# Kernel tuning notes

Measured on AMD Instinct MI355X. Metric: run time of the kernel, lower is better.

The kernel has to match this reference:

```python
import jax, jax.numpy as jnp
import numpy as np

B, S, D, P, H = 32, 1024, 512, 720, 4   # batch, seq_len (=codebook_size), enc_in, pred_len, heads
COMMIT_W, ORTHO_W = 1.0, 0.8


def setup_inputs() -> dict:
    key = jax.random.key(0)
    ks = jax.random.split(key, 6)
    return {
        "x": jax.random.normal(ks[0], (B, S, D), jnp.float32),
        "w_in": jax.random.normal(ks[1], (H * D, D), jnp.float32) * 0.02,   # project_in: dim -> heads*dim
        "b_in": jnp.zeros((H * D,), jnp.float32),
        "embed": jax.random.normal(ks[2], (H, S, D), jnp.float32),          # per-head codebook [h, C, d]
        "w_out": jax.random.normal(ks[3], (D, H * D), jnp.float32) * 0.02,  # project_out: heads*dim -> dim
        "b_out": jnp.zeros((D,), jnp.float32),
        "w_lin": jax.random.normal(ks[4], (P, S), jnp.float32) * 0.02,      # Linear over time axis
        "b_lin": jnp.zeros((P,), jnp.float32),
    }


def reference(x, w_in, b_in, embed, w_out, b_out, w_lin, b_lin):
    C = embed.shape[1]
    # Normalization: subtract last timestep (detached)
    seq_last = jax.lax.stop_gradient(x[:, -1:, :])          # [B,1,D]
    x0 = x - seq_last                                       # [B,S,D]

    # --- VectorQuantize ---
    xi = x0 @ w_in.T + b_in                                 # [B,S,H*D] project_in
    # 'b n (h d) -> h (b n) d' (separate codebook per head)
    f = xi.reshape(B, S, H, D).transpose(2, 0, 1, 3).reshape(H, B * S, D)
    # squared-euclidean distances to codes: [H, B*S, C]
    d2 = (jnp.sum(f * f, -1, keepdims=True)
          - 2.0 * jnp.einsum('hnd,hcd->hnc', f, embed)
          + jnp.sum(embed * embed, -1)[:, None, :])
    ind = jnp.argmin(d2, axis=-1)                           # [H, B*S]
    q = jnp.take_along_axis(embed, ind[:, :, None], axis=1)  # gather -> [H, B*S, D]

    # commitment loss (learnable codebook => quantize NOT detached)
    commit_loss = jnp.mean((q - f) ** 2)
    # orthogonal regularization on full codebook
    normed = embed / jnp.linalg.norm(embed, axis=-1, keepdims=True)
    cs = jnp.einsum('hid,hjd->hij', normed, normed)         # [H,C,C]
    ortho_loss = jnp.sum(cs ** 2) / (H * C * C) - 1.0 / C
    loss = COMMIT_W * commit_loss + ORTHO_W * ortho_loss

    # straight-through estimator
    q_st = f + jax.lax.stop_gradient(q - f)
    # 'h (b n) d -> b n (h d)'
    qo = q_st.reshape(H, B, S, D).transpose(1, 2, 0, 3).reshape(B, S, H * D)
    quantized = qo @ w_out.T + b_out                        # [B,S,D] project_out

    # Linear over the time axis: permute(0,2,1) -> Linear(S->P) -> permute back
    y = jnp.einsum('bnd,pn->bpd', quantized, w_lin) + b_lin[None, :, None]
    y = y + seq_last                                        # [B,P,D]

    indices = ind.reshape(H, B, S).transpose(1, 2, 0)       # [B,S,H]
    return y, indices, loss
```

## Files before the change

kernel.cpp:

```cpp
#include <hip/hip_runtime.h>
#include <stdint.h>

typedef unsigned int u32;
typedef unsigned long long u64;
typedef _Float16 f16;
typedef __attribute__((ext_vector_type(8))) _Float16 f16x8;
typedef __attribute__((ext_vector_type(4))) _Float16 f16x4;
typedef __attribute__((ext_vector_type(2))) _Float16 f16x2;
typedef __attribute__((ext_vector_type(4))) float f32x4;

#define MFMA16(a, b, c) __builtin_amdgcn_mfma_f32_16x16x32_f16((a), (b), (c), 0, 0, 0)
#define MARGIN 2.0f
#define WAITV(n) asm volatile("s_waitcnt vmcnt(" #n ")" ::: "memory")

__device__ __forceinline__ u32 ford(float x) { u32 u = __float_as_uint(x); return (u & 0x80000000u) ? ~u : (u | 0x80000000u); }
__device__ __forceinline__ float iford(u32 v) { u32 u = (v & 0x80000000u) ? (v & 0x7FFFFFFFu) : ~v; return __uint_as_float(u); }
__device__ __forceinline__ int xswz(int i, int n) { return (i & 7) * (n >> 3) + (i >> 3); }

typedef __attribute__((address_space(1))) const unsigned char ga_t;
typedef __attribute__((address_space(3))) unsigned char la_t;
__device__ __forceinline__ void gl16(const void* g, void* l) {
  __builtin_amdgcn_global_load_lds((ga_t*)g, (la_t*)l, 16, 0, 0);
}

__device__ __forceinline__ void stgp(const f16* g, int kt, char* sdst, int tid) {
#pragma unroll
  for (int it = 0; it < 2; ++it) {
    const int u = (tid + (it << 9)) << 4;
    const int r = u >> 7, sl = (u >> 4) & 7;
    const char* src = (const char*)g + (size_t)r * 1024 + ((size_t)kt << 7) +
                      (size_t)((sl ^ (r & 7)) << 4);
    gl16(src, sdst + u);
  }
}

__device__ __forceinline__ f16x8 rdf(const char* bb, int pb, int rr, int ks, int lane) {
  return *(const f16x8*)(bb + pb + rr * 128 +
                         ((((ks << 2) + (lane >> 4)) ^ (rr & 7)) << 4));
}

template <bool ISK1>
__global__ __launch_bounds__(512, 1) void gemm8(
    const f16* __restrict__ A0, const f16* __restrict__ A1,
    const f16* __restrict__ B0, const f16* __restrict__ B1,
    int chrows, void* __restrict__ out0, void* __restrict__ out1,
    const float* __restrict__ bias, const float* __restrict__ aux) {
  __shared__ char lds[131072 + (ISK1 ? 0 : 4096)];
  const int tid = threadIdx.x;
  const int lane = tid & 63, wid = tid >> 6;
  const int wm = wid >> 2, wn = wid & 3;

  int blkm, blkn, z = 0;
  {
    const int s = xswz(blockIdx.x, gridDim.x);
    if constexpr (ISK1) { blkn = s & 15; blkm = s >> 4; }
    else {
      const int bph = (chrows >> 8) << 2;
      z = s / bph;
      const int rem = s - z * bph;
      blkm = rem >> 2; blkn = rem & 3;
    }
  }

  if constexpr (!ISK1) {
    ((int*)(lds + 131072))[tid] = 0;
    ((int*)(lds + 131072))[tid + 512] = 0;
  }

  const f16 *p0, *p1, *p2, *p3;
  if constexpr (ISK1) {
    p0 = A0 + (size_t)blkm * 65536;
    p1 = A1 + (size_t)blkm * 65536;
    p2 = B0 + (size_t)blkn * 65536;
    p3 = B1 + (size_t)blkn * 65536;
  } else {
    p0 = A0 + ((size_t)z * chrows + (size_t)blkm * 256) * 512;
    p1 = p0 + 65536;
    p2 = B0 + (size_t)z * 524288 + (size_t)blkn * 131072;
    p3 = p2 + 65536;
  }

  constexpr int NACC = ISK1 ? 8 : 32;
  f32x4 acc[NACC];
#pragma unroll
  for (int i = 0; i < NACC; ++i) acc[i] = f32x4{0.f, 0.f, 0.f, 0.f};

  stgp(p0, 0, lds + 0, tid);
  stgp(p1, 0, lds + 16384, tid);
  stgp(p2, 0, lds + 32768, tid);
  stgp(p3, 0, lds + 49152, tid);

#pragma unroll
  for (int kc = 0; kc < 8; ++kc) {
    const char* bb = lds + (kc & 1) * 65536;
    char* nb = lds + ((kc + 1) & 1) * 65536;
    __builtin_amdgcn_s_barrier();
    if (kc + 1 < 8) {
      stgp(p0, kc + 1, nb + 0, tid);
      stgp(p1, kc + 1, nb + 16384, tid);
      stgp(p2, kc + 1, nb + 32768, tid);
      stgp(p3, kc + 1, nb + 49152, tid);
      WAITV(8);
    } else {
      WAITV(0);
    }
    __builtin_amdgcn_s_barrier();

    if constexpr (!ISK1) {
      f16x8 a[4][2], b[4][2];
      const int pbA = wm * 16384;
      const int pbB = 32768 + (wn >> 1) * 16384;
      const int rB = (wn & 1) * 64 + (lane & 15);
#pragma unroll
      for (int mt = 0; mt < 4; ++mt)
#pragma unroll
        for (int ks = 0; ks < 2; ++ks) a[mt][ks] = rdf(bb, pbA, mt * 16 + (lane & 15), ks, lane);
#pragma unroll
      for (int nt = 0; nt < 2; ++nt)
#pragma unroll
        for (int ks = 0; ks < 2; ++ks) b[nt][ks] = rdf(bb, pbB, rB + nt * 16, ks, lane);
      __builtin_amdgcn_s_setprio(1);
#pragma unroll
      for (int nt = 0; nt < 2; ++nt)
#pragma unroll
        for (int mt = 0; mt < 4; ++mt)
#pragma unroll
          for (int ks = 0; ks < 2; ++ks) acc[mt * 4 + nt] = MFMA16(a[mt][ks], b[nt][ks], acc[mt * 4 + nt]);
      __builtin_amdgcn_s_setprio(0);
#pragma unroll
      for (int nt = 2; nt < 4; ++nt)
#pragma unroll
        for (int ks = 0; ks < 2; ++ks) b[nt][ks] = rdf(bb, pbB, rB + nt * 16, ks, lane);
      __builtin_amdgcn_s_setprio(1);
#pragma unroll
      for (int nt = 2; nt < 4; ++nt)
#pragma unroll
        for (int mt = 0; mt < 4; ++mt)
#pragma unroll
          for (int ks = 0; ks < 2; ++ks) acc[mt * 4 + nt] = MFMA16(a[mt][ks], b[nt][ks], acc[mt * 4 + nt]);
      __builtin_amdgcn_s_setprio(0);
#pragma unroll
      for (int mt = 0; mt < 4; ++mt)
#pragma unroll
        for (int ks = 0; ks < 2; ++ks) a[mt][ks] = rdf(bb, pbA, (mt + 4) * 16 + (lane & 15), ks, lane);
      __builtin_amdgcn_s_setprio(1);
#pragma unroll
      for (int nt = 2; nt < 4; ++nt)
#pragma unroll
        for (int mt = 0; mt < 4; ++mt)
#pragma unroll
          for (int ks = 0; ks < 2; ++ks) acc[(mt + 4) * 4 + nt] = MFMA16(a[mt][ks], b[nt][ks], acc[(mt + 4) * 4 + nt]);
      __builtin_amdgcn_s_setprio(0);
      __builtin_amdgcn_s_setprio(1);
#pragma unroll
      for (int nt = 0; nt < 2; ++nt)
#pragma unroll
        for (int mt = 0; mt < 4; ++mt)
#pragma unroll
          for (int ks = 0; ks < 2; ++ks) acc[(mt + 4) * 4 + nt] = MFMA16(a[mt][ks], b[nt][ks], acc[(mt + 4) * 4 + nt]);
      __builtin_amdgcn_s_setprio(0);
    } else {
      f16x8 ah[2][2], al[2][2], bh[2][2], bl[2][2];
      const int rA = wm * 64 + (lane & 15);
      const int rB = wn * 32 + (lane & 15);
#pragma unroll
      for (int mt = 0; mt < 2; ++mt)
#pragma unroll
        for (int ks = 0; ks < 2; ++ks) {
          ah[mt][ks] = rdf(bb, 0, rA + mt * 16, ks, lane);
          al[mt][ks] = rdf(bb, 16384, rA + mt * 16, ks, lane);
        }
#pragma unroll
      for (int ks = 0; ks < 2; ++ks) {
        bh[0][ks] = rdf(bb, 32768, rB, ks, lane);
        bl[0][ks] = rdf(bb, 49152, rB, ks, lane);
      }
      __builtin_amdgcn_s_setprio(1);
#pragma unroll
      for (int mt = 0; mt < 2; ++mt)
#pragma unroll
        for (int ks = 0; ks < 2; ++ks) {
          acc[mt * 2] = MFMA16(al[mt][ks], bh[0][ks], acc[mt * 2]);
          acc[mt * 2] = MFMA16(ah[mt][ks], bl[0][ks], acc[mt * 2]);
          acc[mt * 2] = MFMA16(ah[mt][ks], bh[0][ks], acc[mt * 2]);
        }
      __builtin_amdgcn_s_setprio(0);
#pragma unroll
      for (int ks = 0; ks < 2; ++ks) {
        bh[1][ks] = rdf(bb, 32768, rB + 16, ks, lane);
        bl[1][ks] = rdf(bb, 49152, rB + 16, ks, lane);
      }
      __builtin_amdgcn_s_setprio(1);
#pragma unroll
      for (int mt = 0; mt < 2; ++mt)
#pragma unroll
        for (int ks = 0; ks < 2; ++ks) {
          acc[mt * 2 + 1] = MFMA16(al[mt][ks], bh[1][ks], acc[mt * 2 + 1]);
          acc[mt * 2 + 1] = MFMA16(ah[mt][ks], bl[1][ks], acc[mt * 2 + 1]);
          acc[mt * 2 + 1] = MFMA16(ah[mt][ks], bh[1][ks], acc[mt * 2 + 1]);
        }
      __builtin_amdgcn_s_setprio(0);
#pragma unroll
      for (int mt = 0; mt < 2; ++mt)
#pragma unroll
        for (int ks = 0; ks < 2; ++ks) {
          ah[mt][ks] = rdf(bb, 0, rA + (mt + 2) * 16, ks, lane);
          al[mt][ks] = rdf(bb, 16384, rA + (mt + 2) * 16, ks, lane);
        }
      __builtin_amdgcn_s_setprio(1);
#pragma unroll
      for (int mt = 0; mt < 2; ++mt)
#pragma unroll
        for (int ks = 0; ks < 2; ++ks) {
          acc[(mt + 2) * 2 + 1] = MFMA16(al[mt][ks], bh[1][ks], acc[(mt + 2) * 2 + 1]);
          acc[(mt + 2) * 2 + 1] = MFMA16(ah[mt][ks], bl[1][ks], acc[(mt + 2) * 2 + 1]);
          acc[(mt + 2) * 2 + 1] = MFMA16(ah[mt][ks], bh[1][ks], acc[(mt + 2) * 2 + 1]);
        }
      __builtin_amdgcn_s_setprio(0);
      __builtin_amdgcn_s_setprio(1);
#pragma unroll
      for (int mt = 0; mt < 2; ++mt)
#pragma unroll
        for (int ks = 0; ks < 2; ++ks) {
          acc[(mt + 2) * 2] = MFMA16(al[mt][ks], bh[0][ks], acc[(mt + 2) * 2]);
          acc[(mt + 2) * 2] = MFMA16(ah[mt][ks], bl[0][ks], acc[(mt + 2) * 2]);
          acc[(mt + 2) * 2] = MFMA16(ah[mt][ks], bh[0][ks], acc[(mt + 2) * 2]);
        }
      __builtin_amdgcn_s_setprio(0);
    }
  }

  if constexpr (ISK1) {
    f16* fh = (f16*)out0;
    f16* fl = (f16*)out1;
#pragma unroll
    for (int nt = 0; nt < 2; ++nt) {
      const int gc = blkn * 128 + wn * 32 + nt * 16 + (lane & 15);
      const float bv = bias[gc];
      const int h = gc >> 9, d = gc & 511;
#pragma unroll
      for (int mt = 0; mt < 4; ++mt)
#pragma unroll
        for (int r = 0; r < 4; ++r) {
          const int grow = blkm * 128 + wm * 64 + mt * 16 + ((lane >> 4) << 2) + r;
          const float v = acc[mt * 2 + nt][r] * 6.103515625e-05f + bv;
          const f16 hv = (f16)v;
          const size_t off = ((size_t)h * chrows + grow) * 512 + d;
          fh[off] = hv;
          fl[off] = (f16)(v - (float)hv);
        }
    }
  } else {
    int* cntL = (int*)(lds + 131072);
    u64* candG = (u64*)out0;
    const int h = z;
    float escol[4];
    int cc[4];
#pragma unroll
    for (int nt = 0; nt < 4; ++nt) {
      cc[nt] = blkn * 256 + wn * 64 + nt * 16 + (lane & 15);
      escol[nt] = aux[h * 1024 + cc[nt]];
    }
#pragma unroll
    for (int mt = 0; mt < 8; ++mt)
#pragma unroll
      for (int r = 0; r < 4; ++r) {
        const int row_l = wm * 128 + mt * 16 + ((lane >> 4) << 2) + r;
        float vals[4];
        float mn = 3.4e38f;
#pragma unroll
        for (int nt = 0; nt < 4; ++nt) {
          const float v = escol[nt] - 2.0f * acc[mt * 4 + nt][r];
          vals[nt] = v;
          mn = fminf(mn, v);
        }
#pragma unroll
        for (int o = 1; o < 16; o <<= 1) mn = fminf(mn, __shfl_xor(mn, o));
        const float lim = mn + MARGIN;
#pragma unroll
        for (int nt = 0; nt < 4; ++nt)
          if (vals[nt] <= lim) {
            const int p = atomicAdd(&cntL[row_l * 4 + wn], 1);
            if (p < 4) {
              const size_t grow = (size_t)blkm * 256 + row_l;
              candG[((size_t)h * chrows + grow) * 64 + blkn * 16 + wn * 4 + p] =
                  ((u64)ford(vals[nt]) << 32) | (u32)cc[nt];
            }
          }
      }
  }
}

template <int LDK>
__device__ __forceinline__ void stg8k(const f16* gRowBase, int ktile, char* sdst, int tid) {
#pragma unroll
  for (int it = 0; it < 2; ++it) {
    const int u = (tid + (it << 8)) << 4;
    const int r = u >> 6, s = (u >> 4) & 3;
    const char* src = (const char*)gRowBase + (size_t)r * (LDK * 2) + ((size_t)ktile << 6) +
                      (size_t)((s ^ ((r >> 1) & 3)) << 4);
    gl16(src, sdst + u);
  }
}

template <int MODE>
__global__ __launch_bounds__(256, 3) void gemm2(
    const f16* __restrict__ Ah, const f16* __restrict__ Bh,
    void* __restrict__ out0, const float* __restrict__ bias,
    const float* __restrict__ aux, u64* __restrict__ slots) {
  constexpr int LDK = (MODE == 2 || MODE == 4) ? 1024 : 512;
  constexpr int D = 3;
  constexpr int KT = (MODE == 2 || MODE == 4) ? 32 : 16;
  constexpr int BUF = 16384;
  __shared__ char lds[D * BUF];

  const int tid = threadIdx.x;
  const int lane = tid & 63, wid = tid >> 6;
  const int wm = wid >> 1, wn = wid & 1;

  int blkm, blkn, z = 0;
  {
    const int s = xswz(blockIdx.x, gridDim.x);
    if constexpr (MODE == 1) { blkn = s & 3; blkm = s >> 2; z = blkm >> 3; }
    else if constexpr (MODE == 2) { blkn = s & 3; blkm = (s >> 2) & 3; z = s >> 4; }
    else { const int r2 = s % 24; blkm = r2 % 6; blkn = r2 / 6; z = s / 24; }
  }

  const f16 *Ab, *Bb;
  if constexpr (MODE == 1) {
    Ab = Ah + (size_t)blkm * 65536;
    Bb = Bh + (size_t)z * 262144 + (size_t)blkn * 65536;
  } else if constexpr (MODE == 2) {
    Ab = Ah + (size_t)z * 524288 + (size_t)blkm * 131072;
    Bb = Bh + (size_t)z * 524288 + (size_t)blkn * 131072;
  } else {
    Ab = Ah + (size_t)blkm * 131072;
    Bb = Bh + (size_t)z * 524288 + (size_t)blkn * 131072;
  }

  f32x4 acc[4][4];
#pragma unroll
  for (int i = 0; i < 4; ++i)
#pragma unroll
    for (int j = 0; j < 4; ++j) acc[i][j] = f32x4{0.f, 0.f, 0.f, 0.f};

  auto stage = [&](int kt, char* nb) {
    stg8k<LDK>(Ab, kt, nb, tid);
    stg8k<LDK>(Bb, kt, nb + 8192, tid);
  };
#pragma unroll
  for (int d = 0; d < D - 1; ++d) stage(d, lds + d * BUF);

#pragma unroll
  for (int kc = 0; kc < KT; ++kc) {
    if (kc + D - 1 < KT) stage(kc + D - 1, lds + ((kc + D - 1) % D) * BUF);
    const int nf = KT - 1 - kc;
    if (nf >= 2) WAITV(8);
    else if (nf == 1) WAITV(4);
    else WAITV(0);
    __builtin_amdgcn_s_barrier();
    const char* cbuf = lds + (kc % D) * BUF;
    f16x8 ah[4];
#pragma unroll
    for (int mt = 0; mt < 4; ++mt) {
      const int rr = wm * 64 + mt * 16 + (lane & 15);
      ah[mt] = *(const f16x8*)(cbuf + rr * 64 + (((lane >> 4) ^ ((rr >> 1) & 3)) << 4));
    }
    __builtin_amdgcn_s_setprio(1);
#pragma unroll
    for (int nt = 0; nt < 4; ++nt) {
      const int rn = wn * 64 + nt * 16 + (lane & 15);
      const f16x8 bh = *(const f16x8*)(cbuf + 8192 + rn * 64 + (((lane >> 4) ^ ((rn >> 1) & 3)) << 4));
#pragma unroll
      for (int mt = 0; mt < 4; ++mt) acc[mt][nt] = MFMA16(ah[mt], bh, acc[mt][nt]);
    }
    __builtin_amdgcn_s_setprio(0);
    __builtin_amdgcn_s_barrier();
  }

  if constexpr (MODE == 1) {
    f16* o = (f16*)out0;
#pragma unroll
    for (int nt = 0; nt < 4; ++nt) {
      const int gc = blkn * 128 + wn * 64 + nt * 16 + (lane & 15);
#pragma unroll
      for (int mt = 0; mt < 4; ++mt)
#pragma unroll
        for (int r = 0; r < 4; ++r) {
          const size_t grow = (size_t)blkm * 128 + wm * 64 + mt * 16 + ((lane >> 4) << 2) + r;
          o[grow * 512 + gc] = (f16)acc[mt][nt][r];
        }
    }
  } else if constexpr (MODE == 2) {
    float ssum = 0.f;
#pragma unroll
    for (int mt = 0; mt < 4; ++mt)
#pragma unroll
      for (int nt = 0; nt < 4; ++nt)
#pragma unroll
        for (int r = 0; r < 4; ++r) ssum += acc[mt][nt][r] * acc[mt][nt][r];
#pragma unroll
    for (int o = 1; o < 64; o <<= 1) ssum += __shfl_xor(ssum, o);
    float* wp = (float*)lds;
    __syncthreads();
    if (lane == 0) wp[wid] = ssum;
    __syncthreads();
    if (tid == 0) {
      const float p = wp[0] + wp[1] + wp[2] + wp[3];
      atomicAdd(slots + (blockIdx.x & 63), (u64)llrintf(p * 16777216.f));
    }
  } else {
    float* oy = (float*)out0 + (size_t)z * 368640;
    const float* xseq = aux + (size_t)z * 524288 + 523776;
    float sl[4];
    int gd[4];
#pragma unroll
    for (int nt = 0; nt < 4; ++nt) {
      gd[nt] = blkn * 128 + wn * 64 + nt * 16 + (lane & 15);
      sl[nt] = xseq[gd[nt]];
    }
#pragma unroll
    for (int mt = 0; mt < 4; ++mt)
#pragma unroll
      for (int r = 0; r < 4; ++r) {
        const int p = blkm * 128 + wm * 64 + mt * 16 + ((lane >> 4) << 2) + r;
        if (p < 720) {
          const float bp = bias[p];
#pragma unroll
          for (int nt = 0; nt < 4; ++nt) oy[(size_t)p * 512 + gd[nt]] = acc[mt][nt][r] + bp + sl[nt];
        }
      }
  }
}

__global__ __launch_bounds__(256, 4) void rescore_k(
    const u64* __restrict__ candG, const f16* __restrict__ fh,
    const f16* __restrict__ fl, const float* __restrict__ embed,
    int n0, int shCH,
    int* __restrict__ indw, float* __restrict__ indout, u64* __restrict__ cslots) {
  const int tid = threadIdx.x, lane = tid & 63, wid = tid >> 6;
  const int r = blockIdx.x * 4 + wid;
  const int h = r >> shCH, row = r & ((1 << shCH) - 1);
  u64 cu = candG[(size_t)r * 64 + lane];
  u64 mn = cu;
#pragma unroll
  for (int o = 1; o < 64; o <<= 1) { const u64 t = __shfl_xor(mn, o); if (t < mn) mn = t; }
  const float lim = iford((u32)(mn >> 32)) + MARGIN;
  const bool pass = iford((u32)(cu >> 32)) <= lim;
  u64 mask = __ballot(pass);
  float fv[8];
  {
    const size_t fo = (size_t)r * 512 + lane * 8;
    const f16x8 hv = *(const f16x8*)(fh + fo);
    const f16x8 lv = *(const f16x8*)(fl + fo);
#pragma unroll
    for (int j = 0; j < 8; ++j) fv[j] = (float)hv[j] + (float)lv[j];
  }
  double bestd = 1e300;
  int bestc = 0x7FFFFFFF;
  while (mask) {
    const int src = __ffsll((unsigned long long)mask) - 1;
    mask &= mask - 1;
    const int c = (int)(u32)__shfl(cu, src);
    const float* e = embed + ((size_t)h * 1024 + c) * 512 + lane * 8;
    const float4 e0 = *(const float4*)e, e1 = *(const float4*)(e + 4);
    const float ev[8] = {e0.x, e0.y, e0.z, e0.w, e1.x, e1.y, e1.z, e1.w};
    double sd = 0.0;
#pragma unroll
    for (int j = 0; j < 8; ++j) { const double d = (double)fv[j] - (double)ev[j]; sd += d * d; }
#pragma unroll
    for (int o = 1; o < 64; o <<= 1) sd += __shfl_xor(sd, o);
    if (sd < bestd || (sd == bestd && c < bestc)) { bestd = sd; bestc = c; }
  }
  if (lane == 0) {
    const int n = n0 + row;
    indw[(size_t)n * 4 + h] = bestc;
    indout[(size_t)n * 4 + h] = (float)bestc;
    atomicAdd(cslots + (blockIdx.x & 255), (u64)llrint(bestd * 65536.0));
  }
}

__global__ __launch_bounds__(256) void quantize_qT(
    const int* __restrict__ indw, const f16* __restrict__ Ep,
    const float* __restrict__ b_out, f16* __restrict__ qT) {
  const int tid = threadIdx.x;
  const int b = blockIdx.x >> 4, s0 = (blockIdx.x & 15) << 6;
  __shared__ int inds[64][4];
  inds[tid >> 2][tid & 3] = indw[(size_t)(b * 1024 + s0 + (tid >> 2)) * 4 + (tid & 3)];
  __syncthreads();
  const int d0 = tid * 2;
  const float ba0 = b_out[d0], ba1 = b_out[d0 + 1];
  u32 r0[32], r1[32];
  f16 t0 = (f16)0.f, t1 = (f16)0.f;
#pragma unroll
  for (int ss = 0; ss < 64; ++ss) {
    float a0 = ba0, a1 = ba1;
#pragma unroll
    for (int h = 0; h < 4; ++h) {
      const int c = inds[ss][h];
      const f16x2 p = *(const f16x2*)(Ep + (((size_t)h * 1024 + c) * 512 + d0));
      a0 += (float)p[0];
      a1 += (float)p[1];
    }
    const f16 q0 = (f16)a0, q1 = (f16)a1;
    if (ss & 1) {
      f16x2 w0; w0[0] = t0; w0[1] = q0; __builtin_memcpy(&r0[ss >> 1], &w0, 4);
      f16x2 w1; w1[0] = t1; w1[1] = q1; __builtin_memcpy(&r1[ss >> 1], &w1, 4);
    } else { t0 = q0; t1 = q1; }
  }
  const size_t o0 = ((size_t)b * 512 + d0) * 1024 + s0;
#pragma unroll
  for (int i = 0; i < 8; ++i) {
    uint4 v; v.x = r0[4 * i]; v.y = r0[4 * i + 1]; v.z = r0[4 * i + 2]; v.w = r0[4 * i + 3];
    *(uint4*)(qT + o0 + (size_t)i * 8) = v;
  }
  const size_t o1 = o0 + 1024;
#pragma unroll
  for (int i = 0; i < 8; ++i) {
    uint4 v; v.x = r1[4 * i]; v.y = r1[4 * i + 1]; v.z = r1[4 * i + 2]; v.w = r1[4 * i + 3];
    *(uint4*)(qT + o1 + (size_t)i * 8) = v;
  }
}

__global__ __launch_bounds__(256) void prep_x0(const float* __restrict__ x, int n0,
                                               f16* __restrict__ ht, f16* __restrict__ lt) {
  const int id = blockIdx.x * 256 + threadIdx.x;
  const int k8 = id & 63, r = id >> 6;
  const int n = n0 + r, b = n >> 10;
  const float* ap = x + (size_t)n * 512 + k8 * 8;
  const float* sp = x + (size_t)b * 524288 + 523776 + k8 * 8;
  const float4 a0 = *(const float4*)ap, a1 = *(const float4*)(ap + 4);
  const float4 s0 = *(const float4*)sp, s1 = *(const float4*)(sp + 4);
  const float v[8] = {(a0.x - s0.x) * 16.f, (a0.y - s0.y) * 16.f, (a0.z - s0.z) * 16.f,
                      (a0.w - s0.w) * 16.f, (a1.x - s1.x) * 16.f, (a1.y - s1.y) * 16.f,
                      (a1.z - s1.z) * 16.f, (a1.w - s1.w) * 16.f};
  f16x8 hv, lv;
#pragma unroll
  for (int j = 0; j < 8; ++j) { const f16 h = (f16)v[j]; hv[j] = h; lv[j] = (f16)(v[j] - (float)h); }
  const size_t off = (size_t)r * 512 + k8 * 8;
  *(f16x8*)(ht + off) = hv;
  *(f16x8*)(lt + off) = lv;
}

__global__ __launch_bounds__(256) void prep_win(const float* __restrict__ src,
                                                f16* __restrict__ hi, f16* __restrict__ lo) {
  const size_t e = ((size_t)blockIdx.x * 256 + threadIdx.x) * 4;
  const float4 v = *(const float4*)(src + e);
  const float w[4] = {v.x * 1024.f, v.y * 1024.f, v.z * 1024.f, v.w * 1024.f};
  f16x4 hv, lv;
#pragma unroll
  for (int j = 0; j < 4; ++j) { const f16 h = (f16)w[j]; hv[j] = h; lv[j] = (f16)(w[j] - (float)h); }
  *(f16x4*)(hi + e) = hv;
  *(f16x4*)(lo + e) = lv;
}

__global__ __launch_bounds__(256) void prep_embed_k(const float* __restrict__ em,
                                                    f16* __restrict__ ef,
                                                    float* __restrict__ esq,
                                                    float* __restrict__ invn) {
  const int tid = threadIdx.x, lane = tid & 63, wid = tid >> 6;
  const int row = blockIdx.x * 4 + wid;
  const float* er = em + (size_t)row * 512 + lane * 8;
  const float4 a = *(const float4*)er, b = *(const float4*)(er + 4);
  f16x8 v;
  v[0] = (f16)a.x; v[1] = (f16)a.y; v[2] = (f16)a.z; v[3] = (f16)a.w;
  v[4] = (f16)b.x; v[5] = (f16)b.y; v[6] = (f16)b.z; v[7] = (f16)b.w;
  *(f16x8*)(ef + (size_t)row * 512 + lane * 8) = v;
  float s = a.x * a.x + a.y * a.y + a.z * a.z + a.w * a.w +
            b.x * b.x + b.y * b.y + b.z * b.z + b.w * b.w;
#pragma unroll
  for (int o = 1; o < 64; o <<= 1) s += __shfl_xor(s, o);
  if (lane == 0) { esq[row] = s; invn[row] = 1.0f / sqrtf(s); }
}

__global__ __launch_bounds__(256) void prep_wout(const float* __restrict__ src,
                                                 f16* __restrict__ dst) {
  const int id = blockIdx.x * 256 + threadIdx.x;
  const int k8 = id & 63, rg = id >> 6;
  const int d = rg & 511, h = rg >> 9;
  const float* ap = src + (size_t)d * 2048 + h * 512 + k8 * 8;
  const float4 a0 = *(const float4*)ap, a1 = *(const float4*)(ap + 4);
  f16x8 v;
  v[0] = (f16)a0.x; v[1] = (f16)a0.y; v[2] = (f16)a0.z; v[3] = (f16)a0.w;
  v[4] = (f16)a1.x; v[5] = (f16)a1.y; v[6] = (f16)a1.z; v[7] = (f16)a1.w;
  *(f16x8*)(dst + (size_t)h * 262144 + (size_t)d * 512 + k8 * 8) = v;
}

__global__ __launch_bounds__(256) void prep_wlin(const float* __restrict__ src,
                                                 f16* __restrict__ dst) {
  const int id = blockIdx.x * 256 + threadIdx.x;
  const int k8 = id & 127, row = id >> 7;
  float4 a0 = {0.f, 0.f, 0.f, 0.f}, a1 = a0;
  if (row < 720) {
    const float* ap = src + (size_t)row * 1024 + k8 * 8;
    a0 = *(const float4*)ap;
    a1 = *(const float4*)(ap + 4);
  }
  f16x8 v;
  v[0] = (f16)a0.x; v[1] = (f16)a0.y; v[2] = (f16)a0.z; v[3] = (f16)a0.w;
  v[4] = (f16)a1.x; v[5] = (f16)a1.y; v[6] = (f16)a1.z; v[7] = (f16)a1.w;
  *(f16x8*)(dst + (size_t)row * 1024 + k8 * 8) = v;
}

__global__ __launch_bounds__(256) void prep_normT(const float* __restrict__ em,
                                                  const float* __restrict__ invn,
                                                  f16* __restrict__ nT) {
  __shared__ float t[64 * 65];
  const int tid = threadIdx.x;
  const int bx = blockIdx.x;
  const int h = bx >> 7, rem = bx & 127, cb = rem >> 3, db = rem & 7;
  const int c0 = cb * 64, d0 = db * 64;
  const int j = tid & 63, i0 = tid >> 6;
#pragma unroll
  for (int p = 0; p < 16; ++p) {
    const int i = p * 4 + i0;
    t[i * 65 + j] = em[(size_t)h * 524288 + (size_t)(c0 + i) * 512 + d0 + j] * invn[h * 1024 + c0 + i];
  }
  __syncthreads();
#pragma unroll
  for (int p = 0; p < 16; ++p) {
    const int i = p * 4 + i0;
    nT[(size_t)h * 524288 + (size_t)(d0 + i) * 1024 + c0 + j] = (f16)t[j * 65 + i];
  }
}

__global__ void finalize_k(const u64* __restrict__ cs, const u64* __restrict__ gs,
                           float* __restrict__ out) {
  const int lane = threadIdx.x;
  u64 c = cs[lane] + cs[lane + 64] + cs[lane + 128] + cs[lane + 192];
  u64 g = gs[lane];
#pragma unroll
  for (int o = 1; o < 64; o <<= 1) {
    c += __shfl_xor(c, o);
    g += __shfl_xor(g, o);
  }
  if (lane == 0) {
    const double commit = (double)c / 65536.0 / 67108864.0;
    const double ortho = (double)g / 16777216.0 / 4194304.0 - (1.0 / 1024.0);
    out[11927552] = (float)(commit + 0.8 * ortho);
  }
}

__global__ void ws_fail_k(float* out) {
  if (threadIdx.x == 0) out[11927552] = -777777.0f;
}

extern "C" void kernel_launch(void* const* d_in, const int* in_sizes, int n_in,
                              void* d_out, int out_size, void* d_ws, size_t ws_size,
                              hipStream_t stream) {
  (void)in_sizes; (void)n_in; (void)out_size;
  const float* x = (const float*)d_in[0];
  const float* w_in = (const float*)d_in[1];
  const float* b_in = (const float*)d_in[2];
  const float* embed = (const float*)d_in[3];
  const float* w_out = (const float*)d_in[4];
  const float* b_out = (const float*)d_in[5];
  const float* w_lin = (const float*)d_in[6];
  const float* b_lin = (const float*)d_in[7];
  float* out = (float*)d_out;
  char* ws = (char*)d_ws;

  constexpr size_t SZ_WIN = 2097152, SZ_EFT = 4194304, SZ_WOUT = 2097152;
  constexpr size_t SZ_EP = 4194304, SZ_WLIN = 1572864, SZ_NT = 4194304;
  constexpr size_t SZ_SMALL = 16384 + 16384 + 524288 + 2048 + 512;
  constexpr size_t FIXED = SZ_WIN * 2 + SZ_EFT + SZ_WOUT + SZ_EP + SZ_WLIN + SZ_NT + SZ_SMALL;

  int CH = 16384, shCH = 14;
  if (ws_size < FIXED + (size_t)16384 * 12288) { CH = 8192; shCH = 13; }
  if (ws_size < FIXED + (size_t)CH * 12288) {
    ws_fail_k<<<1, 64, 0, stream>>>(out);
    return;
  }

  size_t off = 0;
  f16* x0h = (f16*)(ws + off); off += (size_t)CH * 1024;
  f16* x0l = (f16*)(ws + off); off += (size_t)CH * 1024;
  f16* fh = (f16*)(ws + off); off += (size_t)CH * 4096;
  f16* fl = (f16*)(ws + off); off += (size_t)CH * 4096;
  u64* cand = (u64*)(ws + off); off += (size_t)CH * 2048;
  f16* winh = (f16*)(ws + off); off += SZ_WIN;
  f16* winl = (f16*)(ws + off); off += SZ_WIN;
  f16* eft = (f16*)(ws + off); off += SZ_EFT;
  f16* wout = (f16*)(ws + off); off += SZ_WOUT;
  f16* Ep = (f16*)(ws + off); off += SZ_EP;
  f16* wlint = (f16*)(ws + off); off += SZ_WLIN;
  f16* nT = (f16*)(ws + off); off += SZ_NT;
  float* esq = (float*)(ws + off); off += 16384;
  float* invn = (float*)(ws + off); off += 16384;
  int* indw = (int*)(ws + off); off += 524288;
  u64* cslots = (u64*)(ws + off); off += 2048;
  u64* gslots = (u64*)(ws + off); off += 512;
  f16* qT = (f16*)ws;

  hipMemsetAsync((void*)cslots, 0, 2560, stream);

  prep_win<<<1024, 256, 0, stream>>>(w_in, winh, winl);
  prep_embed_k<<<1024, 256, 0, stream>>>(embed, eft, esq, invn);
  prep_normT<<<512, 256, 0, stream>>>(embed, invn, nT);
  prep_wout<<<512, 256, 0, stream>>>(w_out, wout);
  prep_wlin<<<384, 256, 0, stream>>>(w_lin, wlint);

  gemm2<1><<<128, 256, 0, stream>>>(eft, wout, Ep, nullptr, nullptr, nullptr);
  gemm2<2><<<64, 256, 0, stream>>>(nT, nT, nullptr, nullptr, nullptr, gslots);

  for (int c0 = 0; c0 < 32768; c0 += CH) {
    prep_x0<<<CH / 4, 256, 0, stream>>>(x, c0, x0h, x0l);
    gemm8<true><<<(CH / 128) * 16, 512, 0, stream>>>(x0h, x0l, winh, winl, CH,
                                                     fh, fl, b_in, nullptr);
    hipMemsetAsync((void*)cand, 0xFF, (size_t)CH * 2048, stream);
    gemm8<false><<<(CH / 256) * 16, 512, 0, stream>>>(fh, nullptr, eft, nullptr, CH,
                                                      cand, nullptr, nullptr, esq);
    rescore_k<<<CH, 256, 0, stream>>>(cand, fh, fl, embed, c0, shCH,
                                      indw, out + 11796480, cslots);
  }

  quantize_qT<<<512, 256, 0, stream>>>(indw, Ep, b_out, qT);
  gemm2<4><<<768, 256, 0, stream>>>(wlint, qT, out, b_lin, x, nullptr);
  finalize_k<<<1, 64, 0, stream>>>(cslots, gslots, out);
}
```

Before: 707.7 us.

## Enlarge project-in GEMM tile to 256x256 with 32-wide K steps

The split-precision project-in GEMM (gemm8<true>) moves from 128x128 output tiles with 64-wide K chunks to 256x256 tiles with 32-wide K chunks over 16 iterations. A new staging routine and LDS reader with a matching XOR swizzle handle the narrower rows, and each wave now holds 32 accumulators. The aim is to raise arithmetic intensity and cut redundant global and LDS traffic per output element. In exchange there is more register pressure, twice as many barriers per block, and a quarter as many blocks, which may leave CUs idle.

```diff
diff --git a/kernel.cpp b/kernel.cpp
--- a/kernel.cpp
+++ b/kernel.cpp
@@ -33,10 +33,23 @@
     gl16(src, sdst + u);
   }
 }
-
 __device__ __forceinline__ f16x8 rdf(const char* bb, int pb, int rr, int ks, int lane) {
   return *(const f16x8*)(bb + pb + rr * 128 +
                          ((((ks << 2) + (lane >> 4)) ^ (rr & 7)) << 4));
+}
+
+__device__ __forceinline__ void stg256(const f16* g, int kt, char* sdst, int tid) {
+#pragma unroll
+  for (int it = 0; it < 2; ++it) {
+    const int u = (tid + (it << 9)) << 4;
+    const int r = u >> 6, sl = (u >> 4) & 3;
+    const char* src = (const char*)g + (size_t)r * 1024 + ((size_t)kt << 6) +
+                      (size_t)((sl ^ ((r >> 1) & 3)) << 4);
+    gl16(src, sdst + u);
+  }
+}
+__device__ __forceinline__ f16x8 rd32(const char* bb, int pb, int rr, int lane) {
+  return *(const f16x8*)(bb + pb + rr * 64 + (((lane >> 4) ^ ((rr >> 1) & 3)) << 4));
 }
 
 template <bool ISK1>
@@ -53,7 +66,7 @@
   int blkm, blkn, z = 0;
   {
     const int s = xswz(blockIdx.x, gridDim.x);
-    if constexpr (ISK1) { blkn = s & 15; blkm = s >> 4; }
+    if constexpr (ISK1) { blkn = s & 7; blkm = s >> 3; }
     else {
       const int bph = (chrows >> 8) << 2;
       z = s / bph;
@@ -69,10 +82,10 @@
 
   const f16 *p0, *p1, *p2, *p3;
   if constexpr (ISK1) {
-    p0 = A0 + (size_t)blkm * 65536;
-    p1 = A1 + (size_t)blkm * 65536;
-    p2 = B0 + (size_t)blkn * 65536;
-    p3 = B1 + (size_t)blkn * 65536;
+    p0 = A0 + (size_t)blkm * 131072;
+    p1 = A1 + (size_t)blkm * 131072;
+    p2 = B0 + (size_t)blkn * 131072;
+    p3 = B1 + (size_t)blkn * 131072;
   } else {
     p0 = A0 + ((size_t)z * chrows + (size_t)blkm * 256) * 512;
     p1 = p0 + 65536;
@@ -80,33 +93,116 @@
     p3 = p2 + 65536;
   }
 
-  constexpr int NACC = ISK1 ? 8 : 32;
-  f32x4 acc[NACC];
-#pragma unroll
-  for (int i = 0; i < NACC; ++i) acc[i] = f32x4{0.f, 0.f, 0.f, 0.f};
-
-  stgp(p0, 0, lds + 0, tid);
-  stgp(p1, 0, lds + 16384, tid);
-  stgp(p2, 0, lds + 32768, tid);
-  stgp(p3, 0, lds + 49152, tid);
-
-#pragma unroll
-  for (int kc = 0; kc < 8; ++kc) {
-    const char* bb = lds + (kc & 1) * 65536;
-    char* nb = lds + ((kc + 1) & 1) * 65536;
-    __builtin_amdgcn_s_barrier();
-    if (kc + 1 < 8) {
-      stgp(p0, kc + 1, nb + 0, tid);
-      stgp(p1, kc + 1, nb + 16384, tid);
-      stgp(p2, kc + 1, nb + 32768, tid);
-      stgp(p3, kc + 1, nb + 49152, tid);
-      WAITV(8);
-    } else {
-      WAITV(0);
-    }
-    __builtin_amdgcn_s_barrier();
-
-    if constexpr (!ISK1) {
+  f32x4 acc[32];
+#pragma unroll
+  for (int i = 0; i < 32; ++i) acc[i] = f32x4{0.f, 0.f, 0.f, 0.f};
+
+  if constexpr (ISK1) {
+    stg256(p0, 0, lds + 0, tid);
+    stg256(p1, 0, lds + 16384, tid);
+    stg256(p2, 0, lds + 32768, tid);
+    stg256(p3, 0, lds + 49152, tid);
+#pragma unroll
+    for (int kc = 0; kc < 16; ++kc) {
+      const char* bb = lds + (kc & 1) * 65536;
+      char* nb = lds + ((kc + 1) & 1) * 65536;
+      __builtin_amdgcn_s_barrier();
+      if (kc + 1 < 16) {
+        stg256(p0, kc + 1, nb + 0, tid);
+        stg256(p1, kc + 1, nb + 16384, tid);
+        stg256(p2, kc + 1, nb + 32768, tid);
+        stg256(p3, kc + 1, nb + 49152, tid);
+        WAITV(8);
+      } else {
+        WAITV(0);
+      }
+      __builtin_amdgcn_s_barrier();
+
+      f16x8 ah[4], al[4], bh[4], bl[4];
+      const int rA = wm * 128 + (lane & 15);
+      const int rB = wn * 64 + (lane & 15);
+#pragma unroll
+      for (int mt = 0; mt < 4; ++mt) {
+        ah[mt] = rd32(bb, 0, rA + mt * 16, lane);
+        al[mt] = rd32(bb, 16384, rA + mt * 16, lane);
+      }
+#pragma unroll
+      for (int nt = 0; nt < 2; ++nt) {
+        bh[nt] = rd32(bb, 32768, rB + nt * 16, lane);
+        bl[nt] = rd32(bb, 49152, rB + nt * 16, lane);
+      }
+      __builtin_amdgcn_s_setprio(1);
+#pragma unroll
+      for (int mt = 0; mt < 4; ++mt)
+#pragma unroll
+        for (int nt = 0; nt < 2; ++nt) {
+          acc[mt * 4 + nt] = MFMA16(al[mt], bh[nt], acc[mt * 4 + nt]);
+          acc[mt * 4 + nt] = MFMA16(ah[mt], bl[nt], acc[mt * 4 + nt]);
+          acc[mt * 4 + nt] = MFMA16(ah[mt], bh[nt], acc[mt * 4 + nt]);
+        }
+      __builtin_amdgcn_s_setprio(0);
+#pragma unroll
+      for (int nt = 2; nt < 4; ++nt) {
+        bh[nt] = rd32(bb, 32768, rB + nt * 16, lane);
+        bl[nt] = rd32(bb, 49152, rB + nt * 16, lane);
+      }
+      __builtin_amdgcn_s_setprio(1);
+#pragma unroll
+      for (int mt = 0; mt < 4; ++mt)
+#pragma unroll
+        for (int nt = 2; nt < 4; ++nt) {
+          acc[mt * 4 + nt] = MFMA16(al[mt], bh[nt], acc[mt * 4 + nt]);
+          acc[mt * 4 + nt] = MFMA16(ah[mt], bl[nt], acc[mt * 4 + nt]);
+          acc[mt * 4 + nt] = MFMA16(ah[mt], bh[nt], acc[mt * 4 + nt]);
+        }
+      __builtin_amdgcn_s_setprio(0);
+#pragma unroll
+      for (int mt = 0; mt < 4; ++mt) {
+        ah[mt] = rd32(bb, 0, rA + (mt + 4) * 16, lane);
+        al[mt] = rd32(bb, 16384, rA + (mt + 4) * 16, lane);
+      }
+      __builtin_amdgcn_s_setprio(1);
+#pragma unroll
+      for (int mt = 0; mt < 4; ++mt)
+#pragma unroll
+        for (int nt = 2; nt < 4; ++nt) {
+          acc[(mt + 4) * 4 + nt] = MFMA16(al[mt], bh[nt], acc[(mt + 4) * 4 + nt]);
+          acc[(mt + 4) * 4 + nt] = MFMA16(ah[mt], bl[nt], acc[(mt + 4) * 4 + nt]);
+          acc[(mt + 4) * 4 + nt] = MFMA16(ah[mt], bh[nt], acc[(mt + 4) * 4 + nt]);
+        }
+      __builtin_amdgcn_s_setprio(0);
+      __builtin_amdgcn_s_setprio(1);
+#pragma unroll
+      for (int mt = 0; mt < 4; ++mt)
+#pragma unroll
+        for (int nt = 0; nt < 2; ++nt) {
+          acc[(mt + 4) * 4 + nt] = MFMA16(al[mt], bh[nt], acc[(mt + 4) * 4 + nt]);
+          acc[(mt + 4) * 4 + nt] = MFMA16(ah[mt], bl[nt], acc[(mt + 4) * 4 + nt]);
+          acc[(mt + 4) * 4 + nt] = MFMA16(ah[mt], bh[nt], acc[(mt + 4) * 4 + nt]);
+        }
+      __builtin_amdgcn_s_setprio(0);
+    }
+  } else {
+    stgp(p0, 0, lds + 0, tid);
+    stgp(p1, 0, lds + 16384, tid);
+    stgp(p2, 0, lds + 32768, tid);
+    stgp(p3, 0, lds + 49152, tid);
+#pragma unroll
+    for (int kc = 0; kc < 8; ++kc) {
+      const char* bb = lds + (kc & 1) * 65536;
+      char* nb = lds + ((kc + 1) & 1) * 65536;
+      __builtin_amdgcn_s_barrier();
+      if (kc + 1 < 8) {
+        stgp(p0, kc + 1, nb + 0, tid);
+        stgp(p1, kc + 1, nb + 16384, tid);
+        stgp(p2, kc + 1, nb + 32768, tid);
+        stgp(p3, kc + 1, nb + 49152, tid);
+        WAITV(8);
+      } else {
+        WAITV(0);
+      }
+      __builtin_amdgcn_s_barrier();
+
       f16x8 a[4][2], b[4][2];
       const int pbA = wm * 16384;
       const int pbB = 32768 + (wn >> 1) * 16384;
@@ -159,74 +255,6 @@
 #pragma unroll
           for (int ks = 0; ks < 2; ++ks) acc[(mt + 4) * 4 + nt] = MFMA16(a[mt][ks], b[nt][ks], acc[(mt + 4) * 4 + nt]);
       __builtin_amdgcn_s_setprio(0);
-    } else {
-      f16x8 ah[2][2], al[2][2], bh[2][2], bl[2][2];
-      const int rA = wm * 64 + (lane & 15);
-      const int rB = wn * 32 + (lane & 15);
-#pragma unroll
-      for (int mt = 0; mt < 2; ++mt)
-#pragma unroll
-        for (int ks = 0; ks < 2; ++ks) {
-          ah[mt][ks] = rdf(bb, 0, rA + mt * 16, ks, lane);
-          al[mt][ks] = rdf(bb, 16384, rA + mt * 16, ks, lane);
-        }
-#pragma unroll
-      for (int ks = 0; ks < 2; ++ks) {
-        bh[0][ks] = rdf(bb, 32768, rB, ks, lane);
-        bl[0][ks] = rdf(bb, 49152, rB, ks, lane);
-      }
-      __builtin_amdgcn_s_setprio(1);
-#pragma unroll
-      for (int mt = 0; mt < 2; ++mt)
-#pragma unroll
-        for (int ks = 0; ks < 2; ++ks) {
-          acc[mt * 2] = MFMA16(al[mt][ks], bh[0][ks], acc[mt * 2]);
-          acc[mt * 2] = MFMA16(ah[mt][ks], bl[0][ks], acc[mt * 2]);
-          acc[mt * 2] = MFMA16(ah[mt][ks], bh[0][ks], acc[mt * 2]);
-        }
-      __builtin_amdgcn_s_setprio(0);
-#pragma unroll
-      for (int ks = 0; ks < 2; ++ks) {
-        bh[1][ks] = rdf(bb, 32768, rB + 16, ks, lane);
-        bl[1][ks] = rdf(bb, 49152, rB + 16, ks, lane);
-      }
-      __builtin_amdgcn_s_setprio(1);
-#pragma unroll
-      for (int mt = 0; mt < 2; ++mt)
-#pragma unroll
-        for (int ks = 0; ks < 2; ++ks) {
-          acc[mt * 2 + 1] = MFMA16(al[mt][ks], bh[1][ks], acc[mt * 2 + 1]);
-          acc[mt * 2 + 1] = MFMA16(ah[mt][ks], bl[1][ks], acc[mt * 2 + 1]);
-          acc[mt * 2 + 1] = MFMA16(ah[mt][ks], bh[1][ks], acc[mt * 2 + 1]);
-        }
-      __builtin_amdgcn_s_setprio(0);
-#pragma unroll
-      for (int mt = 0; mt < 2; ++mt)
-#pragma unroll
-        for (int ks = 0; ks < 2; ++ks) {
-          ah[mt][ks] = rdf(bb, 0, rA + (mt + 2) * 16, ks, lane);
-          al[mt][ks] = rdf(bb, 16384, rA + (mt + 2) * 16, ks, lane);
-        }
-      __builtin_amdgcn_s_setprio(1);
-#pragma unroll
-      for (int mt = 0; mt < 2; ++mt)
-#pragma unroll
-        for (int ks = 0; ks < 2; ++ks) {
-          acc[(mt + 2) * 2 + 1] = MFMA16(al[mt][ks], bh[1][ks], acc[(mt + 2) * 2 + 1]);
-          acc[(mt + 2) * 2 + 1] = MFMA16(ah[mt][ks], bl[1][ks], acc[(mt + 2) * 2 + 1]);
-          acc[(mt + 2) * 2 + 1] = MFMA16(ah[mt][ks], bh[1][ks], acc[(mt + 2) * 2 + 1]);
-        }
-      __builtin_amdgcn_s_setprio(0);
-      __builtin_amdgcn_s_setprio(1);
-#pragma unroll
-      for (int mt = 0; mt < 2; ++mt)
-#pragma unroll
-        for (int ks = 0; ks < 2; ++ks) {
-          acc[(mt + 2) * 2] = MFMA16(al[mt][ks], bh[0][ks], acc[(mt + 2) * 2]);
-          acc[(mt + 2) * 2] = MFMA16(ah[mt][ks], bl[0][ks], acc[(mt + 2) * 2]);
-          acc[(mt + 2) * 2] = MFMA16(ah[mt][ks], bh[0][ks], acc[(mt + 2) * 2]);
-        }
-      __builtin_amdgcn_s_setprio(0);
     }
   }
 
@@ -234,16 +262,16 @@
     f16* fh = (f16*)out0;
     f16* fl = (f16*)out1;
 #pragma unroll
-    for (int nt = 0; nt < 2; ++nt) {
-      const int gc = blkn * 128 + wn * 32 + nt * 16 + (lane & 15);
+    for (int nt = 0; nt < 4; ++nt) {
+      const int gc = blkn * 256 + wn * 64 + nt * 16 + (lane & 15);
       const float bv = bias[gc];
       const int h = gc >> 9, d = gc & 511;
 #pragma unroll
-      for (int mt = 0; mt < 4; ++mt)
+      for (int mt = 0; mt < 8; ++mt)
 #pragma unroll
         for (int r = 0; r < 4; ++r) {
-          const int grow = blkm * 128 + wm * 64 + mt * 16 + ((lane >> 4) << 2) + r;
-          const float v = acc[mt * 2 + nt][r] * 6.103515625e-05f + bv;
+          const int grow = blkm * 256 + wm * 128 + mt * 16 + ((lane >> 4) << 2) + r;
+          const float v = acc[mt * 4 + nt][r] * 6.103515625e-05f + bv;
           const f16 hv = (f16)v;
           const size_t off = ((size_t)h * chrows + grow) * 512 + d;
           fh[off] = hv;
@@ -705,8 +733,8 @@
 
   for (int c0 = 0; c0 < 32768; c0 += CH) {
     prep_x0<<<CH / 4, 256, 0, stream>>>(x, c0, x0h, x0l);
-    gemm8<true><<<(CH / 128) * 16, 512, 0, stream>>>(x0h, x0l, winh, winl, CH,
-                                                     fh, fl, b_in, nullptr);
+    gemm8<true><<<(CH / 256) * 8, 512, 0, stream>>>(x0h, x0l, winh, winl, CH,
+                                                    fh, fl, b_in, nullptr);
     hipMemsetAsync((void*)cand, 0xFF, (size_t)CH * 2048, stream);
     gemm8<false><<<(CH / 256) * 16, 512, 0, stream>>>(fh, nullptr, eft, nullptr, CH,
                                                       cand, nullptr, nullptr, esq);
```

New measurement: 743.7 us. 5.1% more time.
